# Kernel tuning notes

Hardware: AMD Instinct MI355X
Metric: run time of the kernel (lower is better)

The kernel has to match this reference:

```python
import jax, jax.numpy as jnp
import numpy as np

BSZ, SEQ, HID, OUT = 32, 2048, 1024, 1024


def setup_inputs() -> dict:
    key = jax.random.key(0)
    k1, k2, k3, k4, k5 = jax.random.split(key, 5)
    hidden = jax.random.normal(k1, (BSZ, HID), dtype=jnp.float32)
    encoder_outs = jax.random.normal(k2, (BSZ, SEQ, OUT), dtype=jnp.float32)
    src_lens = jax.random.randint(k3, (BSZ,), SEQ // 2, SEQ + 1)
    src_lens = src_lens.at[0].set(SEQ)  # ensure max(src_lens) == SEQ as torch code assumes
    # Linear weights init U(-0.1, 0.1), bias=False
    W1 = jax.random.uniform(k4, (OUT, HID), minval=-0.1, maxval=0.1, dtype=jnp.float32)
    W2 = jax.random.uniform(k5, (OUT, HID + OUT), minval=-0.1, maxval=0.1, dtype=jnp.float32)
    return {"hidden": hidden, "encoder_outs": encoder_outs, "src_lens": src_lens,
            "W1": W1, "W2": W2}


def reference(hidden, encoder_outs, src_lens, W1, W2):
    # hidden: [B, H], encoder_outs: [B, S, D], src_lens: [B]
    q = hidden @ W1.T                                      # [B, D]
    att = jnp.einsum('bsd,bd->bs', encoder_outs, q)        # [B, S] scores
    S = encoder_outs.shape[1]
    mask = (jnp.arange(S)[None, :] < src_lens[:, None]).astype(att.dtype)  # [B, S]
    masked = mask * att
    # torch: masked_att[masked_att == 0] = -1e10 (zeros -> large negative before softmax)
    masked = jnp.where(masked == 0, jnp.float32(-1e10), masked)
    attn = jax.nn.softmax(masked, axis=1)                  # softmax over sequence
    ctx = jnp.einsum('bs,bsd->bd', attn, encoder_outs)     # [B, D]
    out = jnp.tanh(jnp.concatenate([ctx, hidden], axis=1) @ W2.T)  # [B, OUT]
    # original returns attn_scores shaped [S, B] (seq-major)
    return out, attn.T
```

## Files before the change

kernel.cpp:

```cpp
#include <hip/hip_runtime.h>
#include <math.h>

#define BSZ 32
#define SEQ 2048
#define HID 1024
#define OUTD 1024
#define K2  (HID + OUTD)

__global__ void q_kernel(const float* __restrict__ hidden,
                         const float* __restrict__ W1,
                         float* __restrict__ q) {
    int gid  = blockIdx.x * blockDim.x + threadIdx.x;
    int wave = gid >> 6;
    int lane = threadIdx.x & 63;
    if (wave >= OUTD * BSZ) return;
    int o = wave >> 5;
    int b = wave & 31;
    const float* w = W1 + (size_t)o * HID;
    const float* h = hidden + (size_t)b * HID;
    float acc = 0.f;
#pragma unroll
    for (int it = 0; it < HID / 256; ++it) {
        int k = it * 256 + lane * 4;
        float4 wv = *reinterpret_cast<const float4*>(w + k);
        float4 hv = *reinterpret_cast<const float4*>(h + k);
        acc += wv.x * hv.x + wv.y * hv.y + wv.z * hv.z + wv.w * hv.w;
    }
#pragma unroll
    for (int off = 32; off; off >>= 1) acc += __shfl_down(acc, off);
    if (lane == 0) q[b * OUTD + o] = acc;
}

__global__ void scores_kernel(const float* __restrict__ enc,
                              const float* __restrict__ q,
                              float* __restrict__ att) {
    int gid  = blockIdx.x * blockDim.x + threadIdx.x;
    int wave = gid >> 6;
    int lane = threadIdx.x & 63;
    if (wave >= BSZ * SEQ) return;
    int b = wave >> 11;
    const float* row = enc + (size_t)wave * HID;
    const float* qb  = q + (size_t)b * OUTD;
    float acc = 0.f;
#pragma unroll
    for (int it = 0; it < HID / 256; ++it) {
        int k = it * 256 + lane * 4;
        float4 e  = *reinterpret_cast<const float4*>(row + k);
        float4 qq = *reinterpret_cast<const float4*>(qb + k);
        acc += e.x * qq.x + e.y * qq.y + e.z * qq.z + e.w * qq.w;
    }
#pragma unroll
    for (int off = 32; off; off >>= 1) acc += __shfl_down(acc, off);
    if (lane == 0) att[wave] = acc;
}

__global__ void softmax_kernel(float* __restrict__ att,
                               const int* __restrict__ src_lens,
                               float* __restrict__ attn_t) {
    int b   = blockIdx.x;
    int len = src_lens[b];
    int tid = threadIdx.x;
    float vals[SEQ / 256];
    float m = -INFINITY;
#pragma unroll
    for (int i = 0; i < SEQ / 256; ++i) {
        int s = tid + i * 256;
        float a = att[b * SEQ + s];
        float masked = (s < len) ? a : 0.f;
        if (masked == 0.f) masked = -1e10f;
        vals[i] = masked;
        m = fmaxf(m, masked);
    }
#pragma unroll
    for (int off = 32; off; off >>= 1) m = fmaxf(m, __shfl_down(m, off));
    __shared__ float sm[4];
    if ((tid & 63) == 0) sm[tid >> 6] = m;
    __syncthreads();
    float bm = fmaxf(fmaxf(sm[0], sm[1]), fmaxf(sm[2], sm[3]));
    float sum = 0.f;
#pragma unroll
    for (int i = 0; i < SEQ / 256; ++i) {
        vals[i] = expf(vals[i] - bm);
        sum += vals[i];
    }
#pragma unroll
    for (int off = 32; off; off >>= 1) sum += __shfl_down(sum, off);
    __shared__ float ss[4];
    if ((tid & 63) == 0) ss[tid >> 6] = sum;
    __syncthreads();
    float inv = 1.f / (ss[0] + ss[1] + ss[2] + ss[3]);
#pragma unroll
    for (int i = 0; i < SEQ / 256; ++i) {
        int s = tid + i * 256;
        float p = vals[i] * inv;
        att[b * SEQ + s]    = p;
        attn_t[s * BSZ + b] = p;
    }
}

#define NCHUNK 32
#define SCHUNK (SEQ / NCHUNK)
__global__ void ctx_kernel(const float* __restrict__ enc,
                           const float* __restrict__ attn,
                           float* __restrict__ ctx) {
    int b     = blockIdx.x >> 5;
    int chunk = blockIdx.x & (NCHUNK - 1);
    int s0    = chunk * SCHUNK;
    int d0    = threadIdx.x * 4;
    const float* base = enc + ((size_t)b * SEQ + s0) * HID + d0;
    float4 acc = make_float4(0.f, 0.f, 0.f, 0.f);
#pragma unroll 4
    for (int i = 0; i < SCHUNK; ++i) {
        float p  = attn[b * SEQ + s0 + i];
        float4 v = *reinterpret_cast<const float4*>(base + (size_t)i * HID);
        acc.x += p * v.x; acc.y += p * v.y; acc.z += p * v.z; acc.w += p * v.w;
    }
    float* c = ctx + b * OUTD + d0;
    atomicAdd(c + 0, acc.x);
    atomicAdd(c + 1, acc.y);
    atomicAdd(c + 2, acc.z);
    atomicAdd(c + 3, acc.w);
}

__global__ void out_kernel(const float* __restrict__ ctx,
                           const float* __restrict__ hidden,
                           const float* __restrict__ W2,
                           float* __restrict__ out) {
    int gid  = blockIdx.x * blockDim.x + threadIdx.x;
    int wave = gid >> 6;
    int lane = threadIdx.x & 63;
    if (wave >= OUTD * BSZ) return;
    int o = wave >> 5;
    int b = wave & 31;
    const float* w = W2 + (size_t)o * K2;
    float acc = 0.f;
#pragma unroll
    for (int it = 0; it < HID / 256; ++it) {
        int k = it * 256 + lane * 4;
        float4 wv = *reinterpret_cast<const float4*>(w + k);
        float4 cv = *reinterpret_cast<const float4*>(ctx + (size_t)b * HID + k);
        acc += wv.x * cv.x + wv.y * cv.y + wv.z * cv.z + wv.w * cv.w;
    }
#pragma unroll
    for (int it = 0; it < HID / 256; ++it) {
        int k = it * 256 + lane * 4;
        float4 wv = *reinterpret_cast<const float4*>(w + HID + k);
        float4 hv = *reinterpret_cast<const float4*>(hidden + (size_t)b * HID + k);
        acc += wv.x * hv.x + wv.y * hv.y + wv.z * hv.z + wv.w * hv.w;
    }
#pragma unroll
    for (int off = 32; off; off >>= 1) acc += __shfl_down(acc, off);
    if (lane == 0) out[b * OUTD + o] = tanhf(acc);
}

extern "C" void kernel_launch(void* const* d_in, const int* in_sizes, int n_in,
                              void* d_out, int out_size, void* d_ws, size_t ws_size,
                              hipStream_t stream) {
    const float* hidden = (const float*)d_in[0];
    const float* enc    = (const float*)d_in[1];
    const int*   lens   = (const int*)d_in[2];
    const float* W1     = (const float*)d_in[3];
    const float* W2     = (const float*)d_in[4];

    float* out    = (float*)d_out;
    float* attn_t = out + BSZ * OUTD;

    float* q   = (float*)d_ws;
    float* att = q + BSZ * OUTD;
    float* ctx = att + BSZ * SEQ;

    hipMemsetAsync(ctx, 0, (size_t)BSZ * OUTD * sizeof(float), stream);

    q_kernel<<<(OUTD * BSZ * 64) / 256, 256, 0, stream>>>(hidden, W1, q);
    scores_kernel<<<(BSZ * SEQ * 64) / 256, 256, 0, stream>>>(enc, q, att);
    softmax_kernel<<<BSZ, 256, 0, stream>>>(att, lens, attn_t);
    ctx_kernel<<<BSZ * NCHUNK, 256, 0, stream>>>(enc, att, ctx);
    out_kernel<<<(OUTD * BSZ * 64) / 256, 256, 0, stream>>>(ctx, hidden, W2, out);
}
```

Measured before the change: 448.9 us.

## Skip masked sequence positions and reuse vectors across outputs in GEMV kernels

The scores and context kernels now read src_lens and skip encoder rows at or beyond each batch's length. Those positions end up with zero softmax weight anyway, so about a quarter of the encoder traffic can be avoided. The q and out GEMV kernels are restructured so each wave keeps its hidden/ctx vector in registers and computes 8 outputs. This cuts redundant vector loads and shrinks the grid. The context kernel also uses 64 sequence chunks instead of 32, which gives more parallelism but doubles the atomic adds.

```diff
diff --git a/kernel.cpp b/kernel.cpp
--- a/kernel.cpp
+++ b/kernel.cpp
@@ -7,38 +7,51 @@
 #define OUTD 1024
 #define K2  (HID + OUTD)
 
+__device__ __forceinline__ float wave_reduce(float v) {
+#pragma unroll
+    for (int off = 32; off; off >>= 1) v += __shfl_down(v, off);
+    return v;
+}
+
 __global__ void q_kernel(const float* __restrict__ hidden,
                          const float* __restrict__ W1,
                          float* __restrict__ q) {
-    int gid  = blockIdx.x * blockDim.x + threadIdx.x;
-    int wave = gid >> 6;
+    int og   = blockIdx.x >> 3;
+    int bg   = blockIdx.x & 7;
+    int wave = threadIdx.x >> 6;
     int lane = threadIdx.x & 63;
-    if (wave >= OUTD * BSZ) return;
-    int o = wave >> 5;
-    int b = wave & 31;
-    const float* w = W1 + (size_t)o * HID;
+    int b    = bg * 4 + wave;
     const float* h = hidden + (size_t)b * HID;
-    float acc = 0.f;
+    float4 hv[4];
 #pragma unroll
-    for (int it = 0; it < HID / 256; ++it) {
-        int k = it * 256 + lane * 4;
-        float4 wv = *reinterpret_cast<const float4*>(w + k);
-        float4 hv = *reinterpret_cast<const float4*>(h + k);
-        acc += wv.x * hv.x + wv.y * hv.y + wv.z * hv.z + wv.w * hv.w;
+    for (int j = 0; j < 4; ++j)
+        hv[j] = *reinterpret_cast<const float4*>(h + j * 256 + lane * 4);
+#pragma unroll
+    for (int oi = 0; oi < 8; ++oi) {
+        int o = og * 8 + oi;
+        const float* w = W1 + (size_t)o * HID;
+        float acc = 0.f;
+#pragma unroll
+        for (int j = 0; j < 4; ++j) {
+            float4 wv = *reinterpret_cast<const float4*>(w + j * 256 + lane * 4);
+            acc += wv.x * hv[j].x + wv.y * hv[j].y + wv.z * hv[j].z + wv.w * hv[j].w;
+        }
+        acc = wave_reduce(acc);
+        if (lane == 0) q[b * OUTD + o] = acc;
     }
-#pragma unroll
-    for (int off = 32; off; off >>= 1) acc += __shfl_down(acc, off);
-    if (lane == 0) q[b * OUTD + o] = acc;
 }
 
 __global__ void scores_kernel(const float* __restrict__ enc,
                               const float* __restrict__ q,
+                              const int* __restrict__ src_lens,
                               float* __restrict__ att) {
     int gid  = blockIdx.x * blockDim.x + threadIdx.x;
     int wave = gid >> 6;
     int lane = threadIdx.x & 63;
     if (wave >= BSZ * SEQ) return;
     int b = wave >> 11;
+    int s = wave & (SEQ - 1);
+    if (s >= src_lens[b]) return;
     const float* row = enc + (size_t)wave * HID;
     const float* qb  = q + (size_t)b * OUTD;
     float acc = 0.f;
@@ -49,8 +62,7 @@
         float4 qq = *reinterpret_cast<const float4*>(qb + k);
         acc += e.x * qq.x + e.y * qq.y + e.z * qq.z + e.w * qq.w;
     }
-#pragma unroll
-    for (int off = 32; off; off >>= 1) acc += __shfl_down(acc, off);
+    acc = wave_reduce(acc);
     if (lane == 0) att[wave] = acc;
 }
 
@@ -83,8 +95,7 @@
         vals[i] = expf(vals[i] - bm);
         sum += vals[i];
     }
-#pragma unroll
-    for (int off = 32; off; off >>= 1) sum += __shfl_down(sum, off);
+    sum = wave_reduce(sum);
     __shared__ float ss[4];
     if ((tid & 63) == 0) ss[tid >> 6] = sum;
     __syncthreads();
@@ -98,19 +109,23 @@
     }
 }
 
-#define NCHUNK 32
+#define NCHUNK 64
 #define SCHUNK (SEQ / NCHUNK)
 __global__ void ctx_kernel(const float* __restrict__ enc,
                            const float* __restrict__ attn,
+                           const int* __restrict__ src_lens,
                            float* __restrict__ ctx) {
-    int b     = blockIdx.x >> 5;
+    int b     = blockIdx.x >> 6;
     int chunk = blockIdx.x & (NCHUNK - 1);
     int s0    = chunk * SCHUNK;
+    int n     = src_lens[b] - s0;
+    if (n <= 0) return;
+    if (n > SCHUNK) n = SCHUNK;
     int d0    = threadIdx.x * 4;
     const float* base = enc + ((size_t)b * SEQ + s0) * HID + d0;
     float4 acc = make_float4(0.f, 0.f, 0.f, 0.f);
 #pragma unroll 4
-    for (int i = 0; i < SCHUNK; ++i) {
+    for (int i = 0; i < n; ++i) {
         float p  = attn[b * SEQ + s0 + i];
         float4 v = *reinterpret_cast<const float4*>(base + (size_t)i * HID);
         acc.x += p * v.x; acc.y += p * v.y; acc.z += p * v.z; acc.w += p * v.w;
@@ -126,31 +141,35 @@
                            const float* __restrict__ hidden,
                            const float* __restrict__ W2,
                            float* __restrict__ out) {
-    int gid  = blockIdx.x * blockDim.x + threadIdx.x;
-    int wave = gid >> 6;
+    int og   = blockIdx.x >> 3;
+    int bg   = blockIdx.x & 7;
+    int wave = threadIdx.x >> 6;
     int lane = threadIdx.x & 63;
-    if (wave >= OUTD * BSZ) return;
-    int o = wave >> 5;
-    int b = wave & 31;
-    const float* w = W2 + (size_t)o * K2;
-    float acc = 0.f;
+    int b    = bg * 4 + wave;
+    float4 cv[4], hv[4];
 #pragma unroll
-    for (int it = 0; it < HID / 256; ++it) {
-        int k = it * 256 + lane * 4;
-        float4 wv = *reinterpret_cast<const float4*>(w + k);
-        float4 cv = *reinterpret_cast<const float4*>(ctx + (size_t)b * HID + k);
-        acc += wv.x * cv.x + wv.y * cv.y + wv.z * cv.z + wv.w * cv.w;
+    for (int j = 0; j < 4; ++j) {
+        cv[j] = *reinterpret_cast<const float4*>(ctx    + (size_t)b * HID + j * 256 + lane * 4);
+        hv[j] = *reinterpret_cast<const float4*>(hidden + (size_t)b * HID + j * 256 + lane * 4);
     }
 #pragma unroll
-    for (int it = 0; it < HID / 256; ++it) {
-        int k = it * 256 + lane * 4;
-        float4 wv = *reinterpret_cast<const float4*>(w + HID + k);
-        float4 hv = *reinterpret_cast<const float4*>(hidden + (size_t)b * HID + k);
-        acc += wv.x * hv.x + wv.y * hv.y + wv.z * hv.z + wv.w * hv.w;
+    for (int oi = 0; oi < 8; ++oi) {
+        int o = og * 8 + oi;
+        const float* w = W2 + (size_t)o * K2;
+        float acc = 0.f;
+#pragma unroll
+        for (int j = 0; j < 4; ++j) {
+            float4 wv = *reinterpret_cast<const float4*>(w + j * 256 + lane * 4);
+            acc += wv.x * cv[j].x + wv.y * cv[j].y + wv.z * cv[j].z + wv.w * cv[j].w;
+        }
+#pragma unroll
+        for (int j = 0; j < 4; ++j) {
+            float4 wv = *reinterpret_cast<const float4*>(w + HID + j * 256 + lane * 4);
+            acc += wv.x * hv[j].x + wv.y * hv[j].y + wv.z * hv[j].z + wv.w * hv[j].w;
+        }
+        acc = wave_reduce(acc);
+        if (lane == 0) out[b * OUTD + o] = tanhf(acc);
     }
-#pragma unroll
-    for (int off = 32; off; off >>= 1) acc += __shfl_down(acc, off);
-    if (lane == 0) out[b * OUTD + o] = tanhf(acc);
 }
 
 extern "C" void kernel_launch(void* const* d_in, const int* in_sizes, int n_in,
@@ -171,9 +190,9 @@
 
     hipMemsetAsync(ctx, 0, (size_t)BSZ * OUTD * sizeof(float), stream);
 
-    q_kernel<<<(OUTD * BSZ * 64) / 256, 256, 0, stream>>>(hidden, W1, q);
-    scores_kernel<<<(BSZ * SEQ * 64) / 256, 256, 0, stream>>>(enc, q, att);
+    q_kernel<<<(OUTD / 8) * (BSZ / 4), 256, 0, stream>>>(hidden, W1, q);
+    scores_kernel<<<(BSZ * SEQ * 64) / 256, 256, 0, stream>>>(enc, q, lens, att);
     softmax_kernel<<<BSZ, 256, 0, stream>>>(att, lens, attn_t);
-    ctx_kernel<<<BSZ * NCHUNK, 256, 0, stream>>>(enc, att, ctx);
-    out_kernel<<<(OUTD * BSZ * 64) / 256, 256, 0, stream>>>(ctx, hidden, W2, out);
+    ctx_kernel<<<BSZ * NCHUNK, 256, 0, stream>>>(enc, att, lens, ctx);
+    out_kernel<<<(OUTD / 8) * (BSZ / 4), 256, 0, stream>>>(ctx, hidden, W2, out);
 }
```

Result: faster. 420.2 us (-6.4%).
